# Kernel tuning notes

Measured on AMD Instinct MI355X. Metric: run time of the kernel, lower is better.

Reference implementation:

```python
import jax, jax.numpy as jnp
import numpy as np

B, T, N, A, D, S, E, H = 32, 64, 16, 20, 128, 32, 64, 256  # batch, time, n_agents, n_actions, state_dim, sample_size, embed_dim, hypernet_embed


def _lin(k, fi, fo):
    return jax.random.normal(k, (fi, fo), jnp.float32) / np.sqrt(fi)


def setup_inputs() -> dict:
    key = jax.random.key(0)
    ks = jax.random.split(key, 16)
    batch = B * T
    states = jax.random.normal(ks[0], (B, T, D), jnp.float32)
    a_idx = jax.random.randint(ks[1], (B, T, N), 0, A)
    actions = jax.nn.one_hot(a_idx, A, dtype=jnp.float32)
    agent_qs = jax.random.normal(ks[2], (B, T, N), jnp.float32)
    max_filter = jnp.zeros((B, T, N), jnp.float32)
    # random agent permutations (torch.multinomial without replacement)
    grand_coalitions = jnp.argsort(jax.random.uniform(ks[3], (batch * S, N)), axis=1).astype(jnp.int32)
    return {
        "states": states, "actions": actions, "agent_qs": agent_qs,
        "max_filter": max_filter, "grand_coalitions": grand_coalitions,
        # hyper_w_1: Linear(D,H) -> ReLU -> Linear(H, E*2A)
        "W1a": _lin(ks[4], D, H), "b1a": jnp.zeros((H,), jnp.float32),
        "W1b": _lin(ks[5], H, E * 2 * A), "b1b": jnp.zeros((E * 2 * A,), jnp.float32),
        # hyper_b_1: Linear(D,E)
        "Wb": _lin(ks[6], D, E), "bb": jnp.zeros((E,), jnp.float32),
        # hyper_w_final: Linear(D,H) -> ReLU -> Linear(H,E)
        "Wfa": _lin(ks[7], D, H), "bfa": jnp.zeros((H,), jnp.float32),
        "Wfb": _lin(ks[8], H, E), "bfb": jnp.zeros((E,), jnp.float32),
        # V: Linear(D,E) -> ReLU -> Linear(E,1)
        "Wv1": _lin(ks[9], D, E), "bv1": jnp.zeros((E,), jnp.float32),
        "Wv2": _lin(ks[10], E, 1), "bv2": jnp.zeros((1,), jnp.float32),
    }


def reference(states, actions, agent_qs, max_filter, grand_coalitions,
              W1a, b1a, W1b, b1b, Wb, bb, Wfa, bfa, Wfb, bfb, Wv1, bv1, Wv2, bv2):
    b, t = states.shape[0], states.shape[1]
    batch = b * t
    n, a = actions.shape[2], actions.shape[3]
    s = grand_coalitions.shape[0] // batch
    e = Wb.shape[1]

    st = states.reshape(batch, -1)                      # [batch, D]
    act = actions.reshape(batch, n, a)                  # [batch, N, A]
    gc = grand_coalitions.reshape(batch, s, n)          # [batch, S, N]

    # individual_map one-hot + tril matmul => subcoalition; mask = sub - ind = (j < gc)
    j = jnp.arange(n)
    sub = (j[None, None, None, :] <= gc[..., None]).astype(st.dtype)   # [batch,S,N,N]
    ind = (j[None, None, None, :] == gc[..., None]).astype(st.dtype)
    mask = sub - ind                                                    # [batch,S,i,j]

    # gathered (permuted) actions: perm_act[b,s,j,:] = act[b, gc[b,s,j], :]
    perm_act = act[jnp.arange(batch)[:, None, None], gc]                # [batch,S,N,A]

    # mean over coalition axis j of masked actions, times coalition size, mean over samples
    numer = jnp.einsum('bsij,bsja->bsia', mask, perm_act)               # sum_j masked actions
    cnt = mask.sum(-1)                                                  # [batch,S,N]
    coal = ((numer / n) * cnt[..., None]).mean(axis=1)                  # [batch,N,A]

    # per (batch, agent) hypernetwork mixing
    inputs = jnp.concatenate([coal, act], axis=-1).reshape(batch * n, 2 * a)  # [bn, 2A]
    st_rep = jnp.broadcast_to(st[:, None, :], (batch, n, st.shape[-1])).reshape(batch * n, -1)

    def mlp2(x, Wa_, ba_, Wb_, bb_):
        return jax.nn.relu(x @ Wa_ + ba_) @ Wb_ + bb_

    w1 = jnp.abs(mlp2(st_rep, W1a, b1a, W1b, b1b)).reshape(-1, 2 * a, e)      # [bn,2A,E]
    b1 = (st_rep @ Wb + bb)                                                   # [bn,E]
    hidden = jax.nn.elu(jnp.einsum('bk,bke->be', inputs, w1) + b1)            # [bn,E]
    w_final = jnp.abs(mlp2(st_rep, Wfa, bfa, Wfb, bfb))                       # [bn,E]
    v = jax.nn.relu(st_rep @ Wv1 + bv1) @ Wv2 + bv2                           # [bn,1]
    y = jnp.sum(hidden * w_final, axis=-1, keepdims=True) + v                 # [bn,1]
    w_est = jnp.abs(y).reshape(b, t, n)

    q_tot = jnp.sum(w_est * agent_qs, axis=2, keepdims=True)                  # [B,T,1]
    return q_tot, w_est
```

## Files before the change

kernel.cpp:

```cpp
#include <hip/hip_runtime.h>
#include <math.h>


#define BATCH 2048

typedef __attribute__((ext_vector_type(8))) short bf16x8;
typedef __attribute__((ext_vector_type(4))) float f32x4;

__device__ inline unsigned short f2bf(float f) {
    unsigned int u = __float_as_uint(f);
    unsigned int r = (u + 0x7FFFu + ((u >> 16) & 1u)) >> 16;
    return (unsigned short)r;
}
__device__ inline float bf2f(unsigned short s) {
    return __uint_as_float(((unsigned int)s) << 16);
}

__global__ __launch_bounds__(256) void k1(
    const float* __restrict__ X,
    const float* __restrict__ W1a, const float* __restrict__ b1a,
    const float* __restrict__ Wfa, const float* __restrict__ bfa,
    const float* __restrict__ Wb,  const float* __restrict__ bb,
    const float* __restrict__ Wv1, const float* __restrict__ bv1,
    const float* __restrict__ W1b,
    unsigned short* __restrict__ h1_bf, float* __restrict__ hf,
    float* __restrict__ b1buf, float* __restrict__ vrelu,
    unsigned short* __restrict__ Bp)
{
    __shared__ float As[16][64];
    __shared__ float Bs[16][64];
    const int t = threadIdx.x, bid = blockIdx.x;

    if (bid >= 320) {
        int idx = (bid - 320) * 256 + t;
        int n_local = idx & 127;
        int g = idx >> 7;
        int kg = g & 3, kcn = g >> 2;
        int kc = kcn & 7, nb = kcn >> 3;
        int kbase = kc * 32 + kg * 8;
        int col = nb * 128 + n_local;
        unsigned short o[8];
        #pragma unroll
        for (int j = 0; j < 8; ++j)
            o[j] = f2bf(W1b[(kbase + j) * 2560 + col]);
        *(uint4*)&Bp[idx * 8] = *(uint4*)o;
        return;
    }

    const int nb = bid % 10, mb = bid / 10;
    const int m0 = mb * 64, n0 = nb * 64;
    const int tx = t & 15, ty = t >> 4;
    const int lm = t >> 2, lk = (t & 3) << 2;
    const int lkk = t >> 4, lnb = (t & 15) << 2;

    const float* Wsrc; const float* bsrc; int ldb, c0;
    if (nb < 4)       { Wsrc = W1a; bsrc = b1a; ldb = 256; c0 = n0; }
    else if (nb < 8)  { Wsrc = Wfa; bsrc = bfa; ldb = 256; c0 = n0 - 256; }
    else if (nb == 8) { Wsrc = Wb;  bsrc = bb;  ldb = 64;  c0 = 0; }
    else              { Wsrc = Wv1; bsrc = bv1; ldb = 64;  c0 = 0; }

    float c[4][4] = {{0}};
    for (int k0 = 0; k0 < 128; k0 += 16) {
        float4 av = *(const float4*)&X[(m0 + lm) * 128 + k0 + lk];
        As[lk][lm] = av.x; As[lk+1][lm] = av.y; As[lk+2][lm] = av.z; As[lk+3][lm] = av.w;
        *(float4*)&Bs[lkk][lnb] = *(const float4*)&Wsrc[(k0 + lkk) * ldb + c0 + lnb];
        __syncthreads();
        #pragma unroll
        for (int kk = 0; kk < 16; ++kk) {
            float4 a4 = *(const float4*)&As[kk][ty * 4];
            float4 b4 = *(const float4*)&Bs[kk][tx * 4];
            float aa[4] = {a4.x, a4.y, a4.z, a4.w};
            float bb4[4] = {b4.x, b4.y, b4.z, b4.w};
            #pragma unroll
            for (int i = 0; i < 4; ++i)
                #pragma unroll
                for (int j = 0; j < 4; ++j)
                    c[i][j] = fmaf(aa[i], bb4[j], c[i][j]);
        }
        __syncthreads();
    }
    const int ncol = c0 + tx * 4;
    float4 bias = *(const float4*)&bsrc[ncol];
    #pragma unroll
    for (int i = 0; i < 4; ++i) {
        int m = m0 + ty * 4 + i;
        float v0 = c[i][0] + bias.x, v1 = c[i][1] + bias.y;
        float v2 = c[i][2] + bias.z, v3 = c[i][3] + bias.w;
        if (nb < 4) {
            ushort4 o;
            o.x = f2bf(fmaxf(v0, 0.f)); o.y = f2bf(fmaxf(v1, 0.f));
            o.z = f2bf(fmaxf(v2, 0.f)); o.w = f2bf(fmaxf(v3, 0.f));
            *(ushort4*)&h1_bf[m * 256 + ncol] = o;
        } else if (nb < 8) {
            float4 o = { fmaxf(v0,0.f), fmaxf(v1,0.f), fmaxf(v2,0.f), fmaxf(v3,0.f) };
            *(float4*)&hf[m * 256 + ncol] = o;
        } else if (nb == 8) {
            float4 o = { v0, v1, v2, v3 };
            *(float4*)&b1buf[m * 64 + ncol] = o;
        } else {
            float4 o = { fmaxf(v0,0.f), fmaxf(v1,0.f), fmaxf(v2,0.f), fmaxf(v3,0.f) };
            *(float4*)&vrelu[m * 64 + ncol] = o;
        }
    }
}

#define AS_STRIDE 40
__global__ __launch_bounds__(256) void k2(
    const unsigned short* __restrict__ A, const unsigned short* __restrict__ Bp,
    const float* __restrict__ bias, unsigned short* __restrict__ C,
    const float* __restrict__ hf, const float* __restrict__ Wfb,
    const float* __restrict__ bfb, float* __restrict__ wf)
{
    __shared__ __align__(16) char smem[18432];
    const int t = threadIdx.x, bid = blockIdx.x;

    if (bid < 320) {
        unsigned short* As = (unsigned short*)smem;
        unsigned short* Bs = (unsigned short*)(smem + 10240);
        const int lane = t & 63, wave = t >> 6;
        const int ln15 = lane & 15, q4 = lane >> 4;
        const int nb = bid % 20, m0 = (bid / 20) * 128, n0 = nb * 128;
        const int wm = (wave & 1) * 64, wn = (wave >> 1) * 64;

        f32x4 acc[4][4];
        #pragma unroll
        for (int i = 0; i < 4; ++i)
            #pragma unroll
            for (int j = 0; j < 4; ++j)
                acc[i][j] = (f32x4){0.f, 0.f, 0.f, 0.f};

        for (int kc = 0; kc < 8; ++kc) {
            #pragma unroll
            for (int c = 0; c < 2; ++c) {
                int ch = t + c * 256;
                int row = ch >> 2, part = ch & 3;
                *(uint4*)&As[row * AS_STRIDE + part * 8] =
                    *(const uint4*)&A[(m0 + row) * 256 + kc * 32 + part * 8];
            }
            {
                const uint4* src = (const uint4*)&Bp[(nb * 8 + kc) * 4096];
                ((uint4*)Bs)[t] = src[t];
                ((uint4*)Bs)[t + 256] = src[t + 256];
            }
            __syncthreads();
            bf16x8 af[4], bfr[4];
            #pragma unroll
            for (int mi = 0; mi < 4; ++mi)
                af[mi] = *(const bf16x8*)&As[(wm + mi * 16 + ln15) * AS_STRIDE + q4 * 8];
            #pragma unroll
            for (int ni = 0; ni < 4; ++ni)
                bfr[ni] = *(const bf16x8*)&Bs[(q4 * 128 + wn + ni * 16 + ln15) * 8];
            #pragma unroll
            for (int mi = 0; mi < 4; ++mi)
                #pragma unroll
                for (int ni = 0; ni < 4; ++ni)
                    acc[mi][ni] = __builtin_amdgcn_mfma_f32_16x16x32_bf16(af[mi], bfr[ni], acc[mi][ni], 0, 0, 0);
            __syncthreads();
        }
        #pragma unroll
        for (int ni = 0; ni < 4; ++ni) {
            int col = n0 + wn + ni * 16 + ln15;
            float bv = bias[col];
            #pragma unroll
            for (int mi = 0; mi < 4; ++mi) {
                #pragma unroll
                for (int j = 0; j < 4; ++j) {
                    int row = m0 + wm + mi * 16 + q4 * 4 + j;
                    C[row * 2560 + col] = f2bf(fabsf(acc[mi][ni][j] + bv));
                }
            }
        }
    } else {
        float* hfs  = (float*)smem;
        float* wfbs = (float*)(smem + 2048);
        const int e = t & 63, mg = t >> 6;
        const int b0 = (bid - 320) * 8;
        float acc0 = 0.f, acc1 = 0.f;

        for (int kc = 0; kc < 4; ++kc) {
            for (int i = t; i < 1024; i += 256)
                ((float4*)wfbs)[i] = ((const float4*)(Wfb + kc * 64 * 64))[i];
            if (t < 128) {
                int r = t >> 4, p = t & 15;
                ((float4*)hfs)[t] = *(const float4*)&hf[(b0 + r) * 256 + kc * 64 + p * 4];
            }
            __syncthreads();
            #pragma unroll 8
            for (int k = 0; k < 64; ++k) {
                float wv = wfbs[k * 64 + e];
                acc0 = fmaf(hfs[mg * 64 + k], wv, acc0);
                acc1 = fmaf(hfs[(mg + 4) * 64 + k], wv, acc1);
            }
            __syncthreads();
        }
        float bf = bfb[e];
        wf[(b0 + mg) * 64 + e]     = fabsf(acc0 + bf);
        wf[(b0 + mg + 4) * 64 + e] = fabsf(acc1 + bf);
    }
}

__global__ __launch_bounds__(1024) void k3(
    const float* __restrict__ actions, const int* __restrict__ gc,
    const unsigned short* __restrict__ w1, const float* __restrict__ b1buf,
    const float* __restrict__ wf, const float* __restrict__ vrelu,
    const float* __restrict__ Wv2, const float* __restrict__ bv2,
    const float* __restrict__ agent_qs, float* __restrict__ out)
{
    __shared__ float ins[16][20];
    __shared__ unsigned short w1s[1280];
    __shared__ int aidx[16];
    __shared__ int q[32][16];
    __shared__ unsigned int msk[32][20];
    __shared__ float wq[16];
    const int t = threadIdx.x, b = blockIdx.x;

    if (t < 160) {
        ((uint4*)w1s)[t] = ((const uint4*)(w1 + b * 2560))[t];
    } else if (t < 480) {
        int u = t - 160;
        float av = actions[b * 320 + u];
        if (av > 0.5f) aidx[u / 20] = u % 20;
    } else if (t < 608) {
        ((uint4*)q)[t - 480] = ((const uint4*)(gc + b * 512))[t - 480];
    } else if (t < 768) {
        ((uint4*)msk)[t - 608] = make_uint4(0u, 0u, 0u, 0u);
    }
    __syncthreads();

    if (t >= 512) {
        int u = t - 512, s = u >> 4, j = u & 15;
        atomicOr(&msk[s][aidx[q[s][j]]], 1u << j);
    }
    __syncthreads();

    if (t < 320) {
        int i = t / 20, a = t % 20;
        float acc = 0.f;
        #pragma unroll 8
        for (int s = 0; s < 32; ++s) {
            int g = q[s][i];
            acc += (float)(g * __popc(msk[s][a] & ((1u << g) - 1u)));
        }
        ins[i][a] = acc * (1.0f / 512.0f);
    }
    __syncthreads();

    const int i = t >> 6, e = t & 63;
    float acc = b1buf[b * 64 + e];
    #pragma unroll
    for (int k = 0; k < 20; ++k)
        acc = fmaf(ins[i][k], bf2f(w1s[k * 64 + e]), acc);
    acc += bf2f(w1[b * 2560 + (20 + aidx[i]) * 64 + e]);
    float hidden = acc > 0.f ? acc : expm1f(acc);
    float p = hidden * wf[b * 64 + e] + vrelu[b * 64 + e] * Wv2[e];
    #pragma unroll
    for (int off = 32; off > 0; off >>= 1)
        p += __shfl_down(p, off, 64);
    if (e == 0) {
        float west = fabsf(p + bv2[0]);
        out[2048 + b * 16 + i] = west;
        wq[i] = west * agent_qs[b * 16 + i];
    }
    __syncthreads();
    if (t == 0) {
        float s = 0.f;
        #pragma unroll
        for (int ii = 0; ii < 16; ++ii) s += wq[ii];
        out[b] = s;
    }
}

extern "C" void kernel_launch(void* const* d_in, const int* in_sizes, int n_in,
                              void* d_out, int out_size, void* d_ws, size_t ws_size,
                              hipStream_t stream) {
    const float* states   = (const float*)d_in[0];
    const float* actions  = (const float*)d_in[1];
    const float* agent_qs = (const float*)d_in[2];
    const int*   gc       = (const int*)d_in[4];
    const float* W1a = (const float*)d_in[5];
    const float* b1a = (const float*)d_in[6];
    const float* W1b = (const float*)d_in[7];
    const float* b1b = (const float*)d_in[8];
    const float* Wb  = (const float*)d_in[9];
    const float* bb  = (const float*)d_in[10];
    const float* Wfa = (const float*)d_in[11];
    const float* bfa = (const float*)d_in[12];
    const float* Wfb = (const float*)d_in[13];
    const float* bfb = (const float*)d_in[14];
    const float* Wv1 = (const float*)d_in[15];
    const float* bv1 = (const float*)d_in[16];
    const float* Wv2 = (const float*)d_in[17];
    const float* bv2 = (const float*)d_in[18];

    float* ws     = (float*)d_ws;
    float* hf     = ws;
    float* b1buf  = hf + 524288;
    float* vrelu  = b1buf + 131072;
    float* wfbuf  = vrelu + 131072;
    unsigned short* h1_bf = (unsigned short*)(wfbuf + 131072);
    unsigned short* Bp    = h1_bf + 524288;
    unsigned short* w1    = Bp + 655360;
    float* out = (float*)d_out;

    k1<<<640, 256, 0, stream>>>(states, W1a, b1a, Wfa, bfa, Wb, bb, Wv1, bv1,
                                W1b, h1_bf, hf, b1buf, vrelu, Bp);
    k2<<<576, 256, 0, stream>>>(h1_bf, Bp, b1b, w1, hf, Wfb, bfb, wfbuf);
    k3<<<BATCH, 1024, 0, stream>>>(actions, gc, w1, b1buf, wfbuf, vrelu,
                                   Wv2, bv2, agent_qs, out);
}
```

Measured before the change: 136.8 us.

## Move coalition computation into first kernel and shrink final kernel blocks

```diff
diff --git a/kernel.cpp b/kernel.cpp
--- a/kernel.cpp
+++ b/kernel.cpp
@@ -23,13 +23,52 @@
     const float* __restrict__ Wb,  const float* __restrict__ bb,
     const float* __restrict__ Wv1, const float* __restrict__ bv1,
     const float* __restrict__ W1b,
+    const float* __restrict__ actions, const int* __restrict__ gc,
     unsigned short* __restrict__ h1_bf, float* __restrict__ hf,
     float* __restrict__ b1buf, float* __restrict__ vrelu,
-    unsigned short* __restrict__ Bp)
+    unsigned short* __restrict__ Bp,
+    float* __restrict__ coal, int* __restrict__ arowbuf)
 {
-    __shared__ float As[16][64];
-    __shared__ float Bs[16][64];
+    __shared__ __align__(16) char smem[8192];
     const int t = threadIdx.x, bid = blockIdx.x;
+
+    if (bid >= 640) {
+        int b = bid - 640;
+        int* q            = (int*)smem;
+        unsigned int* msk = (unsigned int*)(smem + 2048);
+        int* aidx         = (int*)(smem + 2048 + 2560);
+
+        if (t < 128) ((uint4*)q)[t] = ((const uint4*)(gc + b * 512))[t];
+        if (t < 160) ((uint4*)msk)[t] = make_uint4(0u, 0u, 0u, 0u);
+        {
+            float av = actions[b * 320 + t];
+            if (av > 0.5f) aidx[t / 20] = t % 20;
+        }
+        if (t < 64) {
+            float av = actions[b * 320 + 256 + t];
+            if (av > 0.5f) aidx[(256 + t) / 20] = (256 + t) % 20;
+        }
+        __syncthreads();
+        if (t < 16) arowbuf[b * 16 + t] = 20 + aidx[t];
+        {
+            int s = t >> 4, j = t & 15;
+            atomicOr(&msk[s * 20 + aidx[q[s * 16 + j]]], 1u << j);
+            s += 16;
+            atomicOr(&msk[s * 20 + aidx[q[s * 16 + j]]], 1u << j);
+        }
+        __syncthreads();
+        for (int u = t; u < 320; u += 256) {
+            int i = u / 20, a = u % 20;
+            float acc = 0.f;
+            #pragma unroll 8
+            for (int s = 0; s < 32; ++s) {
+                int g = q[s * 16 + i];
+                acc += (float)(g * __popc(msk[s * 20 + a] & ((1u << g) - 1u)));
+            }
+            coal[(b * 16 + i) * 20 + a] = acc * (1.0f / 512.0f);
+        }
+        return;
+    }
 
     if (bid >= 320) {
         int idx = (bid - 320) * 256 + t;
@@ -46,6 +85,9 @@
         *(uint4*)&Bp[idx * 8] = *(uint4*)o;
         return;
     }
+
+    float (*As)[64] = (float(*)[64])smem;
+    float (*Bs)[64] = (float(*)[64])(smem + 4096);
 
     const int nb = bid % 10, mb = bid / 10;
     const int m0 = mb * 64, n0 = nb * 64;
@@ -199,74 +241,61 @@
     }
 }
 
-__global__ __launch_bounds__(1024) void k3(
-    const float* __restrict__ actions, const int* __restrict__ gc,
+__global__ __launch_bounds__(512) void k3(
+    const float* __restrict__ coal, const int* __restrict__ arowbuf,
     const unsigned short* __restrict__ w1, const float* __restrict__ b1buf,
     const float* __restrict__ wf, const float* __restrict__ vrelu,
     const float* __restrict__ Wv2, const float* __restrict__ bv2,
     const float* __restrict__ agent_qs, float* __restrict__ out)
 {
+    __shared__ unsigned short w1s[1280];
     __shared__ float ins[16][20];
-    __shared__ unsigned short w1s[1280];
-    __shared__ int aidx[16];
-    __shared__ int q[32][16];
-    __shared__ unsigned int msk[32][20];
+    __shared__ int arow[16];
     __shared__ float wq[16];
     const int t = threadIdx.x, b = blockIdx.x;
 
     if (t < 160) {
         ((uint4*)w1s)[t] = ((const uint4*)(w1 + b * 2560))[t];
     } else if (t < 480) {
-        int u = t - 160;
-        float av = actions[b * 320 + u];
-        if (av > 0.5f) aidx[u / 20] = u % 20;
-    } else if (t < 608) {
-        ((uint4*)q)[t - 480] = ((const uint4*)(gc + b * 512))[t - 480];
-    } else if (t < 768) {
-        ((uint4*)msk)[t - 608] = make_uint4(0u, 0u, 0u, 0u);
+        ((float*)ins)[t - 160] = coal[b * 320 + (t - 160)];
+    } else if (t < 496) {
+        arow[t - 480] = arowbuf[b * 16 + (t - 480)];
     }
     __syncthreads();
 
-    if (t >= 512) {
-        int u = t - 512, s = u >> 4, j = u & 15;
-        atomicOr(&msk[s][aidx[q[s][j]]], 1u << j);
+    const int e = t & 63, wv = t >> 6;
+    const float b1v = b1buf[b * 64 + e];
+    const float wfv = wf[b * 64 + e];
+    const float vv  = vrelu[b * 64 + e] * Wv2[e];
+    const float b2  = bv2[0];
+
+    #pragma unroll
+    for (int pass = 0; pass < 2; ++pass) {
+        const int i = wv + pass * 8;
+        float acc = b1v;
+        #pragma unroll
+        for (int k = 0; k < 20; ++k)
+            acc = fmaf(ins[i][k], bf2f(w1s[k * 64 + e]), acc);
+        acc += bf2f(w1[b * 2560 + arow[i] * 64 + e]);
+        float hidden = acc > 0.f ? acc : expm1f(acc);
+        float p = hidden * wfv + vv;
+        #pragma unroll
+        for (int off = 32; off > 0; off >>= 1)
+            p += __shfl_down(p, off, 64);
+        if (e == 0) {
+            float west = fabsf(p + b2);
+            out[2048 + b * 16 + i] = west;
+            wq[i] = west * agent_qs[b * 16 + i];
+        }
     }
     __syncthreads();
-
-    if (t < 320) {
-        int i = t / 20, a = t % 20;
-        float acc = 0.f;
-        #pragma unroll 8
-        for (int s = 0; s < 32; ++s) {
-            int g = q[s][i];
-            acc += (float)(g * __popc(msk[s][a] & ((1u << g) - 1u)));
-        }
-        ins[i][a] = acc * (1.0f / 512.0f);
-    }
-    __syncthreads();
-
-    const int i = t >> 6, e = t & 63;
-    float acc = b1buf[b * 64 + e];
-    #pragma unroll
-    for (int k = 0; k < 20; ++k)
-        acc = fmaf(ins[i][k], bf2f(w1s[k * 64 + e]), acc);
-    acc += bf2f(w1[b * 2560 + (20 + aidx[i]) * 64 + e]);
-    float hidden = acc > 0.f ? acc : expm1f(acc);
-    float p = hidden * wf[b * 64 + e] + vrelu[b * 64 + e] * Wv2[e];
-    #pragma unroll
-    for (int off = 32; off > 0; off >>= 1)
-        p += __shfl_down(p, off, 64);
-    if (e == 0) {
-        float west = fabsf(p + bv2[0]);
-        out[2048 + b * 16 + i] = west;
-        wq[i] = west * agent_qs[b * 16 + i];
-    }
-    __syncthreads();
-    if (t == 0) {
-        float s = 0.f;
-        #pragma unroll
-        for (int ii = 0; ii < 16; ++ii) s += wq[ii];
-        out[b] = s;
+    if (t < 16) {
+        float v = wq[t];
+        v += __shfl_down(v, 8, 64);
+        v += __shfl_down(v, 4, 64);
+        v += __shfl_down(v, 2, 64);
+        v += __shfl_down(v, 1, 64);
+        if (t == 0) out[b] = v;
     }
 }
 
@@ -300,11 +329,14 @@
     unsigned short* h1_bf = (unsigned short*)(wfbuf + 131072);
     unsigned short* Bp    = h1_bf + 524288;
     unsigned short* w1    = Bp + 655360;
+    float* coal   = (float*)(w1 + 5242880);
+    int*   arowbuf = (int*)(coal + 655360);
     float* out = (float*)d_out;
 
-    k1<<<640, 256, 0, stream>>>(states, W1a, b1a, Wfa, bfa, Wb, bb, Wv1, bv1,
-                                W1b, h1_bf, hf, b1buf, vrelu, Bp);
+    k1<<<2688, 256, 0, stream>>>(states, W1a, b1a, Wfa, bfa, Wb, bb, Wv1, bv1,
+                                 W1b, actions, gc, h1_bf, hf, b1buf, vrelu, Bp,
+                                 coal, arowbuf);
     k2<<<576, 256, 0, stream>>>(h1_bf, Bp, b1b, w1, hf, Wfb, bfb, wfbuf);
-    k3<<<BATCH, 1024, 0, stream>>>(actions, gc, w1, b1buf, wfbuf, vrelu,
-                                   Wv2, bv2, agent_qs, out);
-}
+    k3<<<BATCH, 512, 0, stream>>>(coal, arowbuf, w1, b1buf, wfbuf, vrelu,
+                                  Wv2, bv2, agent_qs, out);
+}
```

Measured after the change: 132.3 us. -3.3%, faster.
